# Optimization experiments

Hardware: AMD Instinct MI355X
Metric: run time of the kernel (lower is better)

Reference implementation:

```python
import jax, jax.numpy as jnp
import numpy as np

POS_THR = 0.5      # ROI_POSITIVE_THR
NEG_THR = 0.1      # ROI_NEGATIVE_THR
N_SAMPLES = 256    # ROI_SAMPLES
FG_RATIO = 0.25    # ROI_SAMPLE_RATIO
L1W = 1.0          # RPN.L1WEIGHT_INTERSECTION
NUM_FG = int(N_SAMPLES * FG_RATIO)


def _make_boxes(kxy, kwh, shape):
    # valid [x1,y1,x2,y2] boxes in an ~800px image
    xy = jax.random.uniform(kxy, shape[:-1] + (2,)) * 800.0
    wh = jax.random.uniform(kwh, shape[:-1] + (2,)) * 200.0 + 1.0
    return jnp.concatenate([xy, xy + wh], axis=-1)


def setup_inputs() -> dict:
    key = jax.random.key(0)
    k1, k2, k3, k4 = jax.random.split(key, 4)
    proposals = _make_boxes(k1, k2, (16, 16384, 4))  # [B, N, 4]
    gt_boxes = _make_boxes(k3, k4, (16, 128, 4))     # [B, G, 4]
    return {"proposals": proposals, "gt_boxes": gt_boxes}


def _centrehw(b):
    # [x1,y1,x2,y2] -> [cx,cy,w,h]
    x1, y1, x2, y2 = b[..., 0], b[..., 1], b[..., 2], b[..., 3]
    return jnp.stack([(x1 + x2) * 0.5, (y1 + y2) * 0.5, x2 - x1, y2 - y1], axis=-1)


def _targets(gt_c, roi_c):
    dx = (gt_c[..., 0] - roi_c[..., 0]) / roi_c[..., 2]
    dy = (gt_c[..., 1] - roi_c[..., 1]) / roi_c[..., 3]
    dw = jnp.log(gt_c[..., 2] / roi_c[..., 2])
    dh = jnp.log(gt_c[..., 3] / roi_c[..., 3])
    return jnp.stack([dx, dy, dw, dh], axis=-1)


def _iou(prop, gt):
    # prop [B,N,4], gt [B,G,4] -> IoU [B,N,G]
    p = prop[:, :, None, :]
    g = gt[:, None, :, :]
    ix1 = jnp.maximum(p[..., 0], g[..., 0])
    iy1 = jnp.maximum(p[..., 1], g[..., 1])
    ix2 = jnp.minimum(p[..., 2], g[..., 2])
    iy2 = jnp.minimum(p[..., 3], g[..., 3])
    inter = jnp.clip(ix2 - ix1, 0.0) * jnp.clip(iy2 - iy1, 0.0)
    ap = (p[..., 2] - p[..., 0]) * (p[..., 3] - p[..., 1])
    ag = (g[..., 2] - g[..., 0]) * (g[..., 3] - g[..., 1])
    return inter / jnp.maximum(ap + ag - inter, 1e-8)


def _forward(proposals, gt_boxes):
    B, N, _ = proposals.shape
    iou = _iou(proposals, gt_boxes)                       # [B,N,G]
    max_iou = iou.max(axis=-1)                            # [B,N]
    argmax_gt = iou.argmax(axis=-1).astype(jnp.int32)     # [B,N]
    # classify: 1=fg, 0=bg, -1=ignore
    labels = jnp.where(max_iou >= POS_THR, 1,
                       jnp.where(max_iou < NEG_THR, 0, -1)).astype(jnp.int32)
    # randsample: keep <= NUM_FG positives (random), fill rest with negatives.
    r = jax.random.uniform(jax.random.key(1), (B, N))
    pos = labels == 1
    r_pos = jnp.where(pos, r, -1.0)
    order = jnp.argsort(-r_pos, axis=1)
    ranks = jnp.argsort(order, axis=1)                    # rank among positives by r
    pos_sel = pos & (ranks < NUM_FG)
    prio = jnp.where(pos_sel, 3.0 + r,
                     jnp.where(labels == 0, 2.0 + r,
                               jnp.where(pos, 1.0 + r, r)))
    _, idx = jax.lax.top_k(prio, N_SAMPLES)               # [B,S] sampled proposal ids
    batch_labels = jnp.maximum(jnp.take_along_axis(labels, idx, axis=1), 0)  # [B,S]
    roi_batch = jnp.take_along_axis(proposals, idx[..., None], axis=1)       # [B,S,4]
    sel_gt = jnp.take_along_axis(argmax_gt, idx, axis=1)                     # [B,S]
    gt_batch = jnp.take_along_axis(gt_boxes, sel_gt[..., None], axis=1)      # [B,S,4]
    bbox_targets = _targets(_centrehw(gt_batch), _centrehw(roi_batch))       # [B,S,4]
    in_w = jnp.where((batch_labels == 1)[..., None], L1W, 0.0)
    in_w = jnp.broadcast_to(in_w, bbox_targets.shape)
    out_w = (in_w > 0).astype(jnp.float32)
    return roi_batch, batch_labels, bbox_targets, in_w, out_w


def reference(proposals, gt_boxes):
    return _forward(proposals, gt_boxes)
```

## Files before the change

kernel.cpp:

```cpp
#include <hip/hip_runtime.h>
#include <stdint.h>

#define BATCH 16
#define NPROP 16384
#define NGT   128
#define NSAMP 256
#define NFG   64
#define GCAP  512

__device__ __forceinline__ void thr_block(uint32_t c0, uint32_t c1,
                                          uint32_t* o0, uint32_t* o1) {
    const uint32_t k0 = 0u, k1 = 1u, ks2 = 0x1BD11BDBu;
    uint32_t x0 = c0 + k0, x1 = c1 + k1;
#define RND(d) { x0 += x1; x1 = (x1 << d) | (x1 >> (32 - d)); x1 ^= x0; }
    RND(13) RND(15) RND(26) RND(6)   x0 += k1;  x1 += ks2 + 1u;
    RND(17) RND(29) RND(16) RND(24)  x0 += ks2; x1 += k0 + 2u;
    RND(13) RND(15) RND(26) RND(6)   x0 += k0;  x1 += k1 + 3u;
    RND(17) RND(29) RND(16) RND(24)  x0 += k1;  x1 += ks2 + 4u;
    RND(13) RND(15) RND(26) RND(6)   x0 += ks2; x1 += k0 + 5u;
#undef RND
    *o0 = x0; *o1 = x1;
}

__device__ __forceinline__ uint32_t thr_part_xor(uint32_t f) {
    uint32_t a, b; thr_block(0u, f, &a, &b);
    return a ^ b;
}

__global__ void __launch_bounds__(256) k_compute(
    const float* __restrict__ props, const float* __restrict__ gts,
    uint32_t* __restrict__ packed)
{
#pragma clang fp contract(off)
    const int b = blockIdx.y;
    const int n = blockIdx.x * 256 + threadIdx.x;
    __shared__ float4 g4[NGT];
    if (threadIdx.x < NGT)
        g4[threadIdx.x] = ((const float4*)gts)[(size_t)b * NGT + threadIdx.x];
    __syncthreads();
    const float4 pb = ((const float4*)props)[(size_t)b * NPROP + n];
    const float ap = (pb.z - pb.x) * (pb.w - pb.y);
    float best = -1.0f; int bg = 0;
    #pragma unroll 4
    for (int i = 0; i < NGT; ++i) {
        const float4 gb = g4[i];
        float ag = (gb.z - gb.x) * (gb.w - gb.y);
        float w = fmaxf(fminf(pb.z, gb.z) - fmaxf(pb.x, gb.x), 0.0f);
        float h = fmaxf(fminf(pb.w, gb.w) - fmaxf(pb.y, gb.y), 0.0f);
        float inter = w * h;
        float un = fmaxf(ap + ag - inter, 1e-8f);
        float iou = inter / un;
        if (iou > best) { best = iou; bg = i; }
    }
    uint32_t lab = (best >= 0.5f) ? 2u : ((best < 0.1f) ? 1u : 0u);
    const uint32_t f = (uint32_t)b * NPROP + (uint32_t)n;
    packed[f] = ((thr_part_xor(f) >> 9) << 9) | (lab << 7) | (uint32_t)bg;
}

__device__ __forceinline__ float r_from_packed(uint32_t p) {
    return __uint_as_float(0x3F800000u | (p >> 9)) - 1.0f;
}

__device__ __forceinline__ uint64_t keyA(uint32_t p, uint32_t n) {
    return (((uint64_t)(p >> 9)) << 14) | (uint64_t)(16383u - n);
}
__device__ __forceinline__ uint32_t cls_of(uint32_t p, uint32_t n, uint64_t thrA) {
    uint32_t lab = (p >> 7) & 3u;
    if (lab == 2u) return (keyA(p, n) >= thrA) ? 3u : 1u;
    return (lab == 1u) ? 2u : 0u;
}
__device__ __forceinline__ uint64_t keyB(uint32_t p, uint32_t n, uint64_t thrA) {
    float r = r_from_packed(p);
    float prio = (float)cls_of(p, n, thrA) + r;
    return (((uint64_t)__float_as_uint(prio)) << 14) | (uint64_t)(16383u - n);
}

__global__ void __launch_bounds__(1024) k_select(
    const float* __restrict__ props, const float* __restrict__ gts,
    const uint32_t* __restrict__ packed, float* __restrict__ out)
{
#pragma clang fp contract(off)
    const int b = blockIdx.x;
    const int tid = threadIdx.x;
    __shared__ uint4 spk4[NPROP / 4];
    __shared__ uint32_t hist[2048];
    __shared__ uint64_t gat[GCAP];
    __shared__ uint32_t sh_pos, sh_neg, sel_cnt, gcnt;
    __shared__ uint32_t sh_dig, sh_k, sh_cnt_in;
    __shared__ uint64_t sh_thr;
    __shared__ uint64_t sel_keys[NSAMP];
    uint32_t* spk = (uint32_t*)spk4;

    const uint4* pk4 = (const uint4*)(packed + (size_t)b * NPROP);
    if (tid == 0) { sh_pos = 0; sh_neg = 0; sel_cnt = 0; }
    __syncthreads();
    {
        uint32_t cp = 0, cn = 0;
        #pragma unroll
        for (int i = 0; i < 4; i++) {
            uint4 v = pk4[tid + i * 1024];
            spk4[tid + i * 1024] = v;
            cp += (((v.x >> 7) & 3u) == 2u) + (((v.y >> 7) & 3u) == 2u)
                + (((v.z >> 7) & 3u) == 2u) + (((v.w >> 7) & 3u) == 2u);
            cn += (((v.x >> 7) & 3u) == 1u) + (((v.y >> 7) & 3u) == 1u)
                + (((v.z >> 7) & 3u) == 1u) + (((v.w >> 7) & 3u) == 1u);
        }
        #pragma unroll
        for (int off = 32; off > 0; off >>= 1) {
            cp += __shfl_down(cp, off);
            cn += __shfl_down(cn, off);
        }
        if ((tid & 63) == 0) { atomicAdd(&sh_pos, cp); atomicAdd(&sh_neg, cn); }
    }
    __syncthreads();
    const uint32_t npos = sh_pos;
    const uint32_t c3 = (npos < NFG) ? npos : NFG;
    const uint32_t c2 = sh_neg;
    const uint32_t c1 = npos - c3;

    uint64_t thrA = 0, thrB = 0;
    for (int phase = (npos > NFG ? 0 : 1); phase < 2; ++phase) {
        uint32_t k; int shift; uint32_t clsStar = 0;
        if (phase == 0) { k = NFG; shift = 26; }
        else {
            if (NSAMP <= c3 + c2)           { clsStar = 2; k = NSAMP - c3;           shift = 25; }
            else if (NSAMP <= c3 + c2 + c1) { clsStar = 1; k = NSAMP - c3 - c2;      shift = 26; }
            else                            { clsStar = 0; k = NSAMP - c3 - c2 - c1; shift = 34; }
        }
        uint64_t prefix = 0, mask = 0;
        for (;;) {
            hist[tid] = 0; hist[tid + 1024] = 0;
            __syncthreads();
            for (int i = 0; i < 16; i++) {
                uint32_t n = (uint32_t)(tid + i * 1024);
                uint32_t p = spk[n];
                bool elig; uint64_t key;
                if (phase == 0) { elig = (((p >> 7) & 3u) == 2u); key = keyA(p, n); }
                else { elig = (cls_of(p, n, thrA) == clsStar); key = keyB(p, n, thrA); }
                if (elig && ((key ^ prefix) & mask) == 0)
                    atomicAdd(&hist[(uint32_t)(key >> shift) & 2047u], 1u);
            }
            __syncthreads();
            if (tid < 64) {
                const uint32_t lane = tid;
                uint32_t cs = 0;
                if (lane < 32) {
                    const int base = (int)lane * 64;
                    #pragma unroll 8
                    for (int i = 0; i < 64; i++) cs += hist[base + i];
                }
                uint32_t s = cs;
                #pragma unroll
                for (int off = 1; off < 32; off <<= 1) {
                    uint32_t t = __shfl_down(s, off);
                    if (lane + off < 32) s += t;
                }
                uint32_t sExcl = s - cs;
                bool cond = (lane < 32) && (sExcl < k) && (k <= s);
                uint64_t ball = __ballot(cond);
                uint32_t cstar = (uint32_t)(__ffsll((unsigned long long)ball) - 1);
                uint32_t kc = __shfl(k - sExcl, (int)cstar);
                uint32_t val = hist[cstar * 64 + lane];
                uint32_t fi = val;
                #pragma unroll
                for (int off = 1; off < 64; off <<= 1) {
                    uint32_t t = __shfl_down(fi, off);
                    if (lane + off < 64) fi += t;
                }
                uint32_t fExcl = fi - val;
                bool cond2 = (fExcl < kc) && (kc <= fi);
                uint64_t ball2 = __ballot(cond2);
                uint32_t bstar = (uint32_t)(__ffsll((unsigned long long)ball2) - 1);
                if (lane == bstar) {
                    sh_dig = cstar * 64 + lane;
                    sh_k = kc - fExcl;
                    sh_cnt_in = val;
                }
            }
            __syncthreads();
            uint32_t dig = sh_dig, kk = sh_k, cnt = sh_cnt_in;
            prefix |= ((uint64_t)dig) << shift;
            mask   |= 2047ull << shift;
            if (cnt <= GCAP || shift == 0) {
                if (tid == 0) gcnt = 0;
                __syncthreads();
                for (int i = 0; i < 16; i++) {
                    uint32_t n = (uint32_t)(tid + i * 1024);
                    uint32_t p = spk[n];
                    bool elig; uint64_t key;
                    if (phase == 0) { elig = (((p >> 7) & 3u) == 2u); key = keyA(p, n); }
                    else { elig = (cls_of(p, n, thrA) == clsStar); key = keyB(p, n, thrA); }
                    if (elig && ((key ^ prefix) & mask) == 0) {
                        uint32_t s = atomicAdd(&gcnt, 1u);
                        if (s < GCAP) gat[s] = key;
                    }
                }
                __syncthreads();
                uint32_t gc = (gcnt < GCAP) ? gcnt : GCAP;
                if (tid < gc) {
                    uint64_t x = gat[tid];
                    uint32_t r = 0;
                    for (uint32_t j = 0; j < gc; j++) r += (gat[j] > x);
                    if (r == kk - 1) sh_thr = x;
                }
                __syncthreads();
                break;
            } else {
                k = kk;
                shift = (shift >= 11) ? shift - 11 : 0;
                __syncthreads();
            }
        }
        if (phase == 0) thrA = sh_thr; else thrB = sh_thr;
        __syncthreads();
    }

    for (int i = 0; i < 16; i++) {
        uint32_t n = (uint32_t)(tid + i * 1024);
        uint64_t key = keyB(spk[n], n, thrA);
        if (key >= thrB) {
            uint32_t slot = atomicAdd(&sel_cnt, 1u);
            if (slot < NSAMP) sel_keys[slot] = key;
        }
    }
    __syncthreads();

    if (tid < NSAMP) {
        uint64_t x = sel_keys[tid];
        uint32_t r = 0;
        for (int j = 0; j < NSAMP; j++) r += (sel_keys[j] > x);
        uint32_t n = 16383u - (uint32_t)(x & 0x3FFFu);
        uint32_t p = spk[n];
        uint32_t lab = (p >> 7) & 3u;
        uint32_t bg = p & 0x7Fu;
        const float4 pb = ((const float4*)props)[(size_t)b * NPROP + n];
        const float4 gb = ((const float4*)gts)[(size_t)b * NGT + bg];
        const size_t O_ROI = 0;
        const size_t O_LBL = (size_t)BATCH * NSAMP * 4;
        const size_t O_TGT = O_LBL + (size_t)BATCH * NSAMP;
        const size_t O_INW = O_TGT + (size_t)BATCH * NSAMP * 4;
        const size_t O_OUW = O_INW + (size_t)BATCH * NSAMP * 4;
        const size_t row = (size_t)b * NSAMP + r;
        out[O_ROI + row * 4 + 0] = pb.x;
        out[O_ROI + row * 4 + 1] = pb.y;
        out[O_ROI + row * 4 + 2] = pb.z;
        out[O_ROI + row * 4 + 3] = pb.w;
        const int isfg = (lab == 2u) ? 1 : 0;
        out[O_LBL + row] = isfg ? 1.0f : 0.0f;
        float rw  = pb.z - pb.x, rh = pb.w - pb.y;
        float gw  = gb.z - gb.x, gh = gb.w - gb.y;
        out[O_TGT + row * 4 + 0] = ((gb.x + gb.z) * 0.5f - (pb.x + pb.z) * 0.5f) / rw;
        out[O_TGT + row * 4 + 1] = ((gb.y + gb.w) * 0.5f - (pb.y + pb.w) * 0.5f) / rh;
        out[O_TGT + row * 4 + 2] = logf(gw / rw);
        out[O_TGT + row * 4 + 3] = logf(gh / rh);
        float wv = isfg ? 1.0f : 0.0f;
        for (int c = 0; c < 4; c++) {
            out[O_INW + row * 4 + c] = wv;
            out[O_OUW + row * 4 + c] = wv;
        }
    }
}

extern "C" void kernel_launch(void* const* d_in, const int* in_sizes, int n_in,
                              void* d_out, int out_size, void* d_ws, size_t ws_size,
                              hipStream_t stream) {
    (void)in_sizes; (void)n_in; (void)out_size; (void)ws_size;
    const float* props = (const float*)d_in[0];
    const float* gts   = (const float*)d_in[1];
    uint32_t* packed = (uint32_t*)d_ws;
    float* out = (float*)d_out;

    dim3 gridA(NPROP / 256, BATCH);
    k_compute<<<gridA, 256, 0, stream>>>(props, gts, packed);
    k_select<<<BATCH, 1024, 0, stream>>>(props, gts, packed, out);
}
```

Measured before the change: 108.1 us.

## Build first-pass radix histograms in compute kernel via global atomics

The IoU kernel now also builds per-batch 2048-bin histograms for the positive, negative and ignore classes using global atomics, so the select kernel can skip its first histogram pass and read counts directly. The select kernel no longer stages packed data in shared memory and reads it from global/L2 instead. The per-GT area is also precomputed once into shared memory. The cost is a memset plus 262k global atomics, and uncached repeated global reads in the later select passes.

```diff
diff --git a/kernel.cpp b/kernel.cpp
--- a/kernel.cpp
+++ b/kernel.cpp
@@ -29,14 +29,18 @@
 
 __global__ void __launch_bounds__(256) k_compute(
     const float* __restrict__ props, const float* __restrict__ gts,
-    uint32_t* __restrict__ packed)
+    uint32_t* __restrict__ packed, uint32_t* __restrict__ ghist)
 {
 #pragma clang fp contract(off)
     const int b = blockIdx.y;
     const int n = blockIdx.x * 256 + threadIdx.x;
     __shared__ float4 g4[NGT];
-    if (threadIdx.x < NGT)
-        g4[threadIdx.x] = ((const float4*)gts)[(size_t)b * NGT + threadIdx.x];
+    __shared__ float sag[NGT];
+    if (threadIdx.x < NGT) {
+        float4 g = ((const float4*)gts)[(size_t)b * NGT + threadIdx.x];
+        g4[threadIdx.x] = g;
+        sag[threadIdx.x] = (g.z - g.x) * (g.w - g.y);
+    }
     __syncthreads();
     const float4 pb = ((const float4*)props)[(size_t)b * NPROP + n];
     const float ap = (pb.z - pb.x) * (pb.w - pb.y);
@@ -44,17 +48,24 @@
     #pragma unroll 4
     for (int i = 0; i < NGT; ++i) {
         const float4 gb = g4[i];
-        float ag = (gb.z - gb.x) * (gb.w - gb.y);
         float w = fmaxf(fminf(pb.z, gb.z) - fmaxf(pb.x, gb.x), 0.0f);
-        float h = fmaxf(fminf(pb.w, gb.w) - fmaxf(pb.y, gb.y), 0.0f);
-        float inter = w * h;
-        float un = fmaxf(ap + ag - inter, 1e-8f);
+        float hh = fmaxf(fminf(pb.w, gb.w) - fmaxf(pb.y, gb.y), 0.0f);
+        float inter = w * hh;
+        float un = fmaxf(ap + sag[i] - inter, 1e-8f);
         float iou = inter / un;
         if (iou > best) { best = iou; bg = i; }
     }
     uint32_t lab = (best >= 0.5f) ? 2u : ((best < 0.1f) ? 1u : 0u);
     const uint32_t f = (uint32_t)b * NPROP + (uint32_t)n;
-    packed[f] = ((thr_part_xor(f) >> 9) << 9) | (lab << 7) | (uint32_t)bg;
+    uint32_t bits = thr_part_xor(f);
+    packed[f] = ((bits >> 9) << 9) | (lab << 7) | (uint32_t)bg;
+
+    float r = __uint_as_float(0x3F800000u | (bits >> 9)) - 1.0f;
+    uint32_t row, bucket;
+    if (lab == 2u)      { row = 0u; bucket = (bits >> 21) & 2047u; }
+    else if (lab == 1u) { row = 1u; bucket = (__float_as_uint(2.0f + r) >> 11) & 2047u; }
+    else                { row = 2u; bucket = (__float_as_uint(r) >> 20) & 2047u; }
+    atomicAdd(&ghist[(size_t)b * 6144 + row * 2048 + bucket], 1u);
 }
 
 __device__ __forceinline__ float r_from_packed(uint32_t p) {
@@ -77,33 +88,33 @@
 
 __global__ void __launch_bounds__(1024) k_select(
     const float* __restrict__ props, const float* __restrict__ gts,
-    const uint32_t* __restrict__ packed, float* __restrict__ out)
+    const uint32_t* __restrict__ packed, const uint32_t* __restrict__ ghist,
+    float* __restrict__ out)
 {
 #pragma clang fp contract(off)
     const int b = blockIdx.x;
     const int tid = threadIdx.x;
-    __shared__ uint4 spk4[NPROP / 4];
-    __shared__ uint32_t hist[2048];
+    __shared__ uint32_t h[3 * 2048];
+    __shared__ uint32_t hist2[2048];
     __shared__ uint64_t gat[GCAP];
+    __shared__ uint64_t sel_keys[NSAMP];
     __shared__ uint32_t sh_pos, sh_neg, sel_cnt, gcnt;
-    __shared__ uint32_t sh_dig, sh_k, sh_cnt_in;
+    __shared__ uint32_t sh_dig, sh_k, sh_cnt_in, sh_bA, sh_adjSub;
     __shared__ uint64_t sh_thr;
-    __shared__ uint64_t sel_keys[NSAMP];
-    uint32_t* spk = (uint32_t*)spk4;
-
-    const uint4* pk4 = (const uint4*)(packed + (size_t)b * NPROP);
+
+    const uint32_t* pk = packed + (size_t)b * NPROP;
+
     if (tid == 0) { sh_pos = 0; sh_neg = 0; sel_cnt = 0; }
     __syncthreads();
     {
         uint32_t cp = 0, cn = 0;
         #pragma unroll
-        for (int i = 0; i < 4; i++) {
-            uint4 v = pk4[tid + i * 1024];
-            spk4[tid + i * 1024] = v;
-            cp += (((v.x >> 7) & 3u) == 2u) + (((v.y >> 7) & 3u) == 2u)
-                + (((v.z >> 7) & 3u) == 2u) + (((v.w >> 7) & 3u) == 2u);
-            cn += (((v.x >> 7) & 3u) == 1u) + (((v.y >> 7) & 3u) == 1u)
-                + (((v.z >> 7) & 3u) == 1u) + (((v.w >> 7) & 3u) == 1u);
+        for (int i = 0; i < 6; i++) {
+            int idx = tid + i * 1024;
+            uint32_t v = ghist[(size_t)b * 6144 + idx];
+            h[idx] = v;
+            if (i < 2) cp += v;
+            else if (i < 4) cn += v;
         }
         #pragma unroll
         for (int off = 32; off > 0; off >>= 1) {
@@ -120,65 +131,79 @@
 
     uint64_t thrA = 0, thrB = 0;
     for (int phase = (npos > NFG ? 0 : 1); phase < 2; ++phase) {
-        uint32_t k; int shift; uint32_t clsStar = 0;
-        if (phase == 0) { k = NFG; shift = 26; }
+        uint32_t k; int shift; uint32_t clsStar = 0; const uint32_t* hrow;
+        if (phase == 0) { k = NFG; shift = 26; hrow = h; }
         else {
-            if (NSAMP <= c3 + c2)           { clsStar = 2; k = NSAMP - c3;           shift = 25; }
-            else if (NSAMP <= c3 + c2 + c1) { clsStar = 1; k = NSAMP - c3 - c2;      shift = 26; }
-            else                            { clsStar = 0; k = NSAMP - c3 - c2 - c1; shift = 34; }
+            if (NSAMP <= c3 + c2)           { clsStar = 2; k = NSAMP - c3;           shift = 25; hrow = h + 2048; }
+            else if (NSAMP <= c3 + c2 + c1) { clsStar = 1; k = NSAMP - c3 - c2;      shift = 26; hrow = h; }
+            else                            { clsStar = 0; k = NSAMP - c3 - c2 - c1; shift = 34; hrow = h + 4096; }
         }
         uint64_t prefix = 0, mask = 0;
+        bool first = true;
         for (;;) {
-            hist[tid] = 0; hist[tid + 1024] = 0;
-            __syncthreads();
-            for (int i = 0; i < 16; i++) {
-                uint32_t n = (uint32_t)(tid + i * 1024);
-                uint32_t p = spk[n];
-                bool elig; uint64_t key;
-                if (phase == 0) { elig = (((p >> 7) & 3u) == 2u); key = keyA(p, n); }
-                else { elig = (cls_of(p, n, thrA) == clsStar); key = keyB(p, n, thrA); }
-                if (elig && ((key ^ prefix) & mask) == 0)
-                    atomicAdd(&hist[(uint32_t)(key >> shift) & 2047u], 1u);
+            if (!first) {
+                hist2[tid] = 0; hist2[tid + 1024] = 0;
+                __syncthreads();
+                for (int i = 0; i < 16; i++) {
+                    uint32_t n = (uint32_t)(tid + i * 1024);
+                    uint32_t p = pk[n];
+                    bool elig; uint64_t key;
+                    if (phase == 0) { elig = (((p >> 7) & 3u) == 2u); key = keyA(p, n); }
+                    else { elig = (cls_of(p, n, thrA) == clsStar); key = keyB(p, n, thrA); }
+                    if (elig && ((key ^ prefix) & mask) == 0)
+                        atomicAdd(&hist2[(uint32_t)(key >> shift) & 2047u], 1u);
+                }
+                __syncthreads();
             }
-            __syncthreads();
-            if (tid < 64) {
-                const uint32_t lane = tid;
-                uint32_t cs = 0;
-                if (lane < 32) {
-                    const int base = (int)lane * 64;
-                    #pragma unroll 8
-                    for (int i = 0; i < 64; i++) cs += hist[base + i];
-                }
-                uint32_t s = cs;
-                #pragma unroll
-                for (int off = 1; off < 32; off <<= 1) {
-                    uint32_t t = __shfl_down(s, off);
-                    if (lane + off < 32) s += t;
-                }
-                uint32_t sExcl = s - cs;
-                bool cond = (lane < 32) && (sExcl < k) && (k <= s);
-                uint64_t ball = __ballot(cond);
-                uint32_t cstar = (uint32_t)(__ffsll((unsigned long long)ball) - 1);
-                uint32_t kc = __shfl(k - sExcl, (int)cstar);
-                uint32_t val = hist[cstar * 64 + lane];
-                uint32_t fi = val;
-                #pragma unroll
-                for (int off = 1; off < 64; off <<= 1) {
-                    uint32_t t = __shfl_down(fi, off);
-                    if (lane + off < 64) fi += t;
-                }
-                uint32_t fExcl = fi - val;
-                bool cond2 = (fExcl < kc) && (kc <= fi);
-                uint64_t ball2 = __ballot(cond2);
-                uint32_t bstar = (uint32_t)(__ffsll((unsigned long long)ball2) - 1);
-                if (lane == bstar) {
-                    sh_dig = cstar * 64 + lane;
-                    sh_k = kc - fExcl;
-                    sh_cnt_in = val;
+            {
+                const uint32_t* hsrc = first ? hrow : hist2;
+                const bool adj = first && (phase == 1) && (clsStar == 1u);
+                const uint32_t adjB = sh_bA, adjSub = sh_adjSub;
+                if (tid < 64) {
+                    const uint32_t lane = tid;
+                    auto HV = [&](uint32_t d) -> uint32_t {
+                        uint32_t v = hsrc[d];
+                        if (adj) v = (d > adjB) ? 0u : (d == adjB ? v - adjSub : v);
+                        return v;
+                    };
+                    uint32_t cs = 0;
+                    if (lane < 32) {
+                        const uint32_t base = lane * 64u;
+                        #pragma unroll 8
+                        for (uint32_t i = 0; i < 64; i++) cs += HV(base + i);
+                    }
+                    uint32_t s = cs;
+                    #pragma unroll
+                    for (int off = 1; off < 32; off <<= 1) {
+                        uint32_t t = __shfl_down(s, off);
+                        if (lane + off < 32) s += t;
+                    }
+                    uint32_t sExcl = s - cs;
+                    bool cond = (lane < 32) && (sExcl < k) && (k <= s);
+                    uint64_t ball = __ballot(cond);
+                    uint32_t cstar = (uint32_t)(__ffsll((unsigned long long)ball) - 1);
+                    uint32_t kc = __shfl(k - sExcl, (int)cstar);
+                    uint32_t val = HV(cstar * 64u + lane);
+                    uint32_t fi = val;
+                    #pragma unroll
+                    for (int off = 1; off < 64; off <<= 1) {
+                        uint32_t t = __shfl_down(fi, off);
+                        if (lane + off < 64) fi += t;
+                    }
+                    uint32_t fExcl = fi - val;
+                    bool cond2 = (fExcl < kc) && (kc <= fi);
+                    uint64_t ball2 = __ballot(cond2);
+                    uint32_t bstar = (uint32_t)(__ffsll((unsigned long long)ball2) - 1);
+                    if (lane == bstar) {
+                        sh_dig = cstar * 64u + lane;
+                        sh_k = kc - fExcl;
+                        sh_cnt_in = val;
+                    }
                 }
             }
             __syncthreads();
             uint32_t dig = sh_dig, kk = sh_k, cnt = sh_cnt_in;
+            if (phase == 0 && first && tid == 0) { sh_bA = dig; sh_adjSub = kk; }
             prefix |= ((uint64_t)dig) << shift;
             mask   |= 2047ull << shift;
             if (cnt <= GCAP || shift == 0) {
@@ -186,7 +211,7 @@
                 __syncthreads();
                 for (int i = 0; i < 16; i++) {
                     uint32_t n = (uint32_t)(tid + i * 1024);
-                    uint32_t p = spk[n];
+                    uint32_t p = pk[n];
                     bool elig; uint64_t key;
                     if (phase == 0) { elig = (((p >> 7) & 3u) == 2u); key = keyA(p, n); }
                     else { elig = (cls_of(p, n, thrA) == clsStar); key = keyB(p, n, thrA); }
@@ -197,7 +222,7 @@
                 }
                 __syncthreads();
                 uint32_t gc = (gcnt < GCAP) ? gcnt : GCAP;
-                if (tid < gc) {
+                if (tid < (int)gc) {
                     uint64_t x = gat[tid];
                     uint32_t r = 0;
                     for (uint32_t j = 0; j < gc; j++) r += (gat[j] > x);
@@ -208,6 +233,7 @@
             } else {
                 k = kk;
                 shift = (shift >= 11) ? shift - 11 : 0;
+                first = false;
                 __syncthreads();
             }
         }
@@ -217,7 +243,7 @@
 
     for (int i = 0; i < 16; i++) {
         uint32_t n = (uint32_t)(tid + i * 1024);
-        uint64_t key = keyB(spk[n], n, thrA);
+        uint64_t key = keyB(pk[n], n, thrA);
         if (key >= thrB) {
             uint32_t slot = atomicAdd(&sel_cnt, 1u);
             if (slot < NSAMP) sel_keys[slot] = key;
@@ -230,7 +256,7 @@
         uint32_t r = 0;
         for (int j = 0; j < NSAMP; j++) r += (sel_keys[j] > x);
         uint32_t n = 16383u - (uint32_t)(x & 0x3FFFu);
-        uint32_t p = spk[n];
+        uint32_t p = pk[n];
         uint32_t lab = (p >> 7) & 3u;
         uint32_t bg = p & 0x7Fu;
         const float4 pb = ((const float4*)props)[(size_t)b * NPROP + n];
@@ -268,9 +294,11 @@
     const float* props = (const float*)d_in[0];
     const float* gts   = (const float*)d_in[1];
     uint32_t* packed = (uint32_t*)d_ws;
+    uint32_t* ghist  = packed + (size_t)BATCH * NPROP;
     float* out = (float*)d_out;
 
+    hipMemsetAsync(ghist, 0, (size_t)BATCH * 3 * 2048 * sizeof(uint32_t), stream);
     dim3 gridA(NPROP / 256, BATCH);
-    k_compute<<<gridA, 256, 0, stream>>>(props, gts, packed);
-    k_select<<<BATCH, 1024, 0, stream>>>(props, gts, packed, out);
-}
+    k_compute<<<gridA, 256, 0, stream>>>(props, gts, packed, ghist);
+    k_select<<<BATCH, 1024, 0, stream>>>(props, gts, packed, ghist, out);
+}
```

New measurement: 146.1 us. +35.2%, slower.

## Compact pos/neg proposals into per-batch lists and split IoU across thread pairs

Applied to the files above, without the earlier changes.

The compute kernel now splits the 128 GT comparisons across two threads per proposal and precomputes GT areas in shared memory. It also stream-compacts proposals into a per-batch 64-bit entry list, with fg/bg at the front and ignored ones at the back, using wave ballots and global atomic counters. The select kernel then runs its radix top-k only over the compacted front list held in LDS, instead of scanning all 16384 entries per phase. This adds a zeroing kernel launch, global atomics and nondeterministic list order, and a global-memory fallback when the list exceeds LDS capacity.

```diff
diff --git a/kernel.cpp b/kernel.cpp
--- a/kernel.cpp
+++ b/kernel.cpp
@@ -7,6 +7,9 @@
 #define NSAMP 256
 #define NFG   64
 #define GCAP  512
+#define LCAP  8192
+
+typedef unsigned long long ull;
 
 __device__ __forceinline__ void thr_block(uint32_t c0, uint32_t c1,
                                           uint32_t* o0, uint32_t* o1) {
@@ -27,212 +30,258 @@
     return a ^ b;
 }
 
+__global__ void k_zero(uint32_t* c) {
+    if (threadIdx.x < 48) c[threadIdx.x] = 0u;
+}
+
 __global__ void __launch_bounds__(256) k_compute(
     const float* __restrict__ props, const float* __restrict__ gts,
-    uint32_t* __restrict__ packed)
+    ull* __restrict__ lists, uint32_t* __restrict__ cnts)
 {
 #pragma clang fp contract(off)
     const int b = blockIdx.y;
-    const int n = blockIdx.x * 256 + threadIdx.x;
+    const int tid = threadIdx.x;
+    const int half = tid & 1;
+    const int n = blockIdx.x * 128 + (tid >> 1);
     __shared__ float4 g4[NGT];
-    if (threadIdx.x < NGT)
-        g4[threadIdx.x] = ((const float4*)gts)[(size_t)b * NGT + threadIdx.x];
+    __shared__ float sag[NGT];
+    if (tid < NGT) {
+        float4 g = ((const float4*)gts)[(size_t)b * NGT + tid];
+        g4[tid] = g;
+        sag[tid] = (g.z - g.x) * (g.w - g.y);
+    }
     __syncthreads();
     const float4 pb = ((const float4*)props)[(size_t)b * NPROP + n];
     const float ap = (pb.z - pb.x) * (pb.w - pb.y);
     float best = -1.0f; int bg = 0;
+    const int gbase = half << 6;
     #pragma unroll 4
-    for (int i = 0; i < NGT; ++i) {
-        const float4 gb = g4[i];
-        float ag = (gb.z - gb.x) * (gb.w - gb.y);
-        float w = fmaxf(fminf(pb.z, gb.z) - fmaxf(pb.x, gb.x), 0.0f);
-        float h = fmaxf(fminf(pb.w, gb.w) - fmaxf(pb.y, gb.y), 0.0f);
-        float inter = w * h;
-        float un = fmaxf(ap + ag - inter, 1e-8f);
+    for (int i = 0; i < 64; ++i) {
+        const int gi = gbase + i;
+        const float4 gb = g4[gi];
+        float w  = fmaxf(fminf(pb.z, gb.z) - fmaxf(pb.x, gb.x), 0.0f);
+        float hh = fmaxf(fminf(pb.w, gb.w) - fmaxf(pb.y, gb.y), 0.0f);
+        float inter = w * hh;
+        float un = fmaxf(ap + sag[gi] - inter, 1e-8f);
         float iou = inter / un;
-        if (iou > best) { best = iou; bg = i; }
-    }
+        if (iou > best) { best = iou; bg = gi; }
+    }
+    float ob = __shfl_xor(best, 1);
+    int  obg = __shfl_xor(bg, 1);
+    if ((tid & 1) == 0 && ob > best) { best = ob; bg = obg; }
+
     uint32_t lab = (best >= 0.5f) ? 2u : ((best < 0.1f) ? 1u : 0u);
     const uint32_t f = (uint32_t)b * NPROP + (uint32_t)n;
-    packed[f] = ((thr_part_xor(f) >> 9) << 9) | (lab << 7) | (uint32_t)bg;
-}
-
-__device__ __forceinline__ float r_from_packed(uint32_t p) {
-    return __uint_as_float(0x3F800000u | (p >> 9)) - 1.0f;
-}
-
-__device__ __forceinline__ uint64_t keyA(uint32_t p, uint32_t n) {
-    return (((uint64_t)(p >> 9)) << 14) | (uint64_t)(16383u - n);
-}
-__device__ __forceinline__ uint32_t cls_of(uint32_t p, uint32_t n, uint64_t thrA) {
-    uint32_t lab = (p >> 7) & 3u;
-    if (lab == 2u) return (keyA(p, n) >= thrA) ? 3u : 1u;
-    return (lab == 1u) ? 2u : 0u;
-}
-__device__ __forceinline__ uint64_t keyB(uint32_t p, uint32_t n, uint64_t thrA) {
-    float r = r_from_packed(p);
-    float prio = (float)cls_of(p, n, thrA) + r;
-    return (((uint64_t)__float_as_uint(prio)) << 14) | (uint64_t)(16383u - n);
+    uint32_t mant = thr_part_xor(f) >> 9;
+    ull entry = ((ull)(lab == 2u) << 44) | ((ull)mant << 21)
+              | ((ull)(16383u - (uint32_t)n) << 7) | (ull)(uint32_t)bg;
+
+    const bool isEven = (tid & 1) == 0;
+    bool front = isEven && (lab != 0u);
+    bool back  = isEven && (lab == 0u);
+    bool ispos = isEven && (lab == 2u);
+    ull mF = __ballot(front), mB = __ballot(back), mP = __ballot(ispos);
+    uint32_t lane = (uint32_t)tid & 63u;
+    ull lt = lane ? (~0ull >> (64u - lane)) : 0ull;
+    uint32_t bf = 0, bb = 0;
+    if (lane == 0) {
+        if (mF) bf = atomicAdd(&cnts[b],      (uint32_t)__popcll(mF));
+        if (mB) bb = atomicAdd(&cnts[16 + b], (uint32_t)__popcll(mB));
+        if (mP)      atomicAdd(&cnts[32 + b], (uint32_t)__popcll(mP));
+    }
+    bf = (uint32_t)__shfl((int)bf, 0);
+    bb = (uint32_t)__shfl((int)bb, 0);
+    ull* Lb = lists + (size_t)b * NPROP;
+    if (front) Lb[bf + (uint32_t)__popcll(mF & lt)] = entry;
+    if (back)  Lb[16383u - (bb + (uint32_t)__popcll(mB & lt))] = entry;
 }
 
 __global__ void __launch_bounds__(1024) k_select(
     const float* __restrict__ props, const float* __restrict__ gts,
-    const uint32_t* __restrict__ packed, float* __restrict__ out)
+    const ull* __restrict__ lists, const uint32_t* __restrict__ cnts,
+    float* __restrict__ out)
 {
 #pragma clang fp contract(off)
     const int b = blockIdx.x;
     const int tid = threadIdx.x;
-    __shared__ uint4 spk4[NPROP / 4];
+    __shared__ ull      sf[LCAP];
     __shared__ uint32_t hist[2048];
-    __shared__ uint64_t gat[GCAP];
-    __shared__ uint32_t sh_pos, sh_neg, sel_cnt, gcnt;
-    __shared__ uint32_t sh_dig, sh_k, sh_cnt_in;
-    __shared__ uint64_t sh_thr;
-    __shared__ uint64_t sel_keys[NSAMP];
-    uint32_t* spk = (uint32_t*)spk4;
-
-    const uint4* pk4 = (const uint4*)(packed + (size_t)b * NPROP);
-    if (tid == 0) { sh_pos = 0; sh_neg = 0; sel_cnt = 0; }
+    __shared__ ull      gat[GCAP];
+    __shared__ ull      selk[NSAMP];
+    __shared__ uint32_t sela[NSAMP];
+    __shared__ uint32_t sh_dig, sh_k, sh_cnt_in, gcnt, selc;
+    __shared__ ull sh_thr;
+
+    const ull* Lb = lists + (size_t)b * NPROP;
+    const uint32_t npn  = cnts[b];
+    const uint32_t nig  = cnts[16 + b];
+    const uint32_t npos = cnts[32 + b];
+    const bool inLDS = (npn <= LCAP);
+    if (inLDS) for (uint32_t j = tid; j < npn; j += 1024) sf[j] = Lb[j];
+    if (tid == 0) selc = 0;
     __syncthreads();
-    {
-        uint32_t cp = 0, cn = 0;
-        #pragma unroll
-        for (int i = 0; i < 4; i++) {
-            uint4 v = pk4[tid + i * 1024];
-            spk4[tid + i * 1024] = v;
-            cp += (((v.x >> 7) & 3u) == 2u) + (((v.y >> 7) & 3u) == 2u)
-                + (((v.z >> 7) & 3u) == 2u) + (((v.w >> 7) & 3u) == 2u);
-            cn += (((v.x >> 7) & 3u) == 1u) + (((v.y >> 7) & 3u) == 1u)
-                + (((v.z >> 7) & 3u) == 1u) + (((v.w >> 7) & 3u) == 1u);
-        }
-        #pragma unroll
-        for (int off = 32; off > 0; off >>= 1) {
-            cp += __shfl_down(cp, off);
-            cn += __shfl_down(cn, off);
-        }
-        if ((tid & 63) == 0) { atomicAdd(&sh_pos, cp); atomicAdd(&sh_neg, cn); }
-    }
-    __syncthreads();
-    const uint32_t npos = sh_pos;
-    const uint32_t c3 = (npos < NFG) ? npos : NFG;
-    const uint32_t c2 = sh_neg;
-    const uint32_t c1 = npos - c3;
-
-    uint64_t thrA = 0, thrB = 0;
-    for (int phase = (npos > NFG ? 0 : 1); phase < 2; ++phase) {
-        uint32_t k; int shift; uint32_t clsStar = 0;
-        if (phase == 0) { k = NFG; shift = 26; }
-        else {
-            if (NSAMP <= c3 + c2)           { clsStar = 2; k = NSAMP - c3;           shift = 25; }
-            else if (NSAMP <= c3 + c2 + c1) { clsStar = 1; k = NSAMP - c3 - c2;      shift = 26; }
-            else                            { clsStar = 0; k = NSAMP - c3 - c2 - c1; shift = 34; }
-        }
-        uint64_t prefix = 0, mask = 0;
+
+    auto getF = [&](uint32_t j) -> ull { return inLDS ? sf[j] : Lb[j]; };
+    auto keyA_of = [&](ull e) -> ull {
+        return (((e >> 21) & 0x7FFFFFull) << 14) | ((e >> 7) & 0x3FFFull);
+    };
+
+    auto locate = [&](uint32_t k) {
+        if (tid < 64) {
+            const uint32_t lane = (uint32_t)tid;
+            uint32_t cs = 0;
+            if (lane < 32) {
+                const uint32_t base = lane * 64u;
+                #pragma unroll 8
+                for (uint32_t i = 0; i < 64; i++) cs += hist[base + i];
+            }
+            uint32_t s = cs;
+            #pragma unroll
+            for (int off = 1; off < 32; off <<= 1) {
+                uint32_t t = __shfl_down(s, off);
+                if (lane + off < 32) s += t;
+            }
+            uint32_t sExcl = s - cs;
+            bool cond = (lane < 32) && (sExcl < k) && (k <= s);
+            ull ball = __ballot(cond);
+            uint32_t cstar = (uint32_t)(__ffsll((unsigned long long)ball) - 1);
+            uint32_t kc = (uint32_t)__shfl((int)(k - sExcl), (int)cstar);
+            uint32_t val = hist[cstar * 64u + lane];
+            uint32_t fi = val;
+            #pragma unroll
+            for (int off = 1; off < 64; off <<= 1) {
+                uint32_t t = __shfl_down(fi, off);
+                if (lane + off < 64) fi += t;
+            }
+            uint32_t fExcl = fi - val;
+            bool cond2 = (fExcl < kc) && (kc <= fi);
+            ull ball2 = __ballot(cond2);
+            uint32_t bstar = (uint32_t)(__ffsll((unsigned long long)ball2) - 1);
+            if (lane == bstar) {
+                sh_dig = cstar * 64u + lane;
+                sh_k = kc - fExcl;
+                sh_cnt_in = val;
+            }
+        }
+    };
+
+    auto radix = [&](auto&& kf, uint32_t m, uint32_t k, int shift) -> ull {
+        ull prefix = 0, mask = 0;
         for (;;) {
             hist[tid] = 0; hist[tid + 1024] = 0;
             __syncthreads();
-            for (int i = 0; i < 16; i++) {
-                uint32_t n = (uint32_t)(tid + i * 1024);
-                uint32_t p = spk[n];
-                bool elig; uint64_t key;
-                if (phase == 0) { elig = (((p >> 7) & 3u) == 2u); key = keyA(p, n); }
-                else { elig = (cls_of(p, n, thrA) == clsStar); key = keyB(p, n, thrA); }
-                if (elig && ((key ^ prefix) & mask) == 0)
+            for (uint32_t j = tid; j < m; j += 1024) {
+                bool e; ull key = kf(j, e);
+                if (e && ((key ^ prefix) & mask) == 0)
                     atomicAdd(&hist[(uint32_t)(key >> shift) & 2047u], 1u);
             }
             __syncthreads();
-            if (tid < 64) {
-                const uint32_t lane = tid;
-                uint32_t cs = 0;
-                if (lane < 32) {
-                    const int base = (int)lane * 64;
-                    #pragma unroll 8
-                    for (int i = 0; i < 64; i++) cs += hist[base + i];
-                }
-                uint32_t s = cs;
-                #pragma unroll
-                for (int off = 1; off < 32; off <<= 1) {
-                    uint32_t t = __shfl_down(s, off);
-                    if (lane + off < 32) s += t;
-                }
-                uint32_t sExcl = s - cs;
-                bool cond = (lane < 32) && (sExcl < k) && (k <= s);
-                uint64_t ball = __ballot(cond);
-                uint32_t cstar = (uint32_t)(__ffsll((unsigned long long)ball) - 1);
-                uint32_t kc = __shfl(k - sExcl, (int)cstar);
-                uint32_t val = hist[cstar * 64 + lane];
-                uint32_t fi = val;
-                #pragma unroll
-                for (int off = 1; off < 64; off <<= 1) {
-                    uint32_t t = __shfl_down(fi, off);
-                    if (lane + off < 64) fi += t;
-                }
-                uint32_t fExcl = fi - val;
-                bool cond2 = (fExcl < kc) && (kc <= fi);
-                uint64_t ball2 = __ballot(cond2);
-                uint32_t bstar = (uint32_t)(__ffsll((unsigned long long)ball2) - 1);
-                if (lane == bstar) {
-                    sh_dig = cstar * 64 + lane;
-                    sh_k = kc - fExcl;
-                    sh_cnt_in = val;
-                }
-            }
+            locate(k);
             __syncthreads();
             uint32_t dig = sh_dig, kk = sh_k, cnt = sh_cnt_in;
-            prefix |= ((uint64_t)dig) << shift;
+            prefix |= ((ull)dig) << shift;
             mask   |= 2047ull << shift;
             if (cnt <= GCAP || shift == 0) {
                 if (tid == 0) gcnt = 0;
                 __syncthreads();
-                for (int i = 0; i < 16; i++) {
-                    uint32_t n = (uint32_t)(tid + i * 1024);
-                    uint32_t p = spk[n];
-                    bool elig; uint64_t key;
-                    if (phase == 0) { elig = (((p >> 7) & 3u) == 2u); key = keyA(p, n); }
-                    else { elig = (cls_of(p, n, thrA) == clsStar); key = keyB(p, n, thrA); }
-                    if (elig && ((key ^ prefix) & mask) == 0) {
+                for (uint32_t j = tid; j < m; j += 1024) {
+                    bool e; ull key = kf(j, e);
+                    if (e && ((key ^ prefix) & mask) == 0) {
                         uint32_t s = atomicAdd(&gcnt, 1u);
                         if (s < GCAP) gat[s] = key;
                     }
                 }
                 __syncthreads();
                 uint32_t gc = (gcnt < GCAP) ? gcnt : GCAP;
-                if (tid < gc) {
-                    uint64_t x = gat[tid];
+                if (tid < (int)gc) {
+                    ull x = gat[tid];
                     uint32_t r = 0;
                     for (uint32_t j = 0; j < gc; j++) r += (gat[j] > x);
                     if (r == kk - 1) sh_thr = x;
                 }
                 __syncthreads();
-                break;
+                return sh_thr;
             } else {
                 k = kk;
                 shift = (shift >= 11) ? shift - 11 : 0;
                 __syncthreads();
             }
         }
-        if (phase == 0) thrA = sh_thr; else thrB = sh_thr;
-        __syncthreads();
-    }
-
-    for (int i = 0; i < 16; i++) {
-        uint32_t n = (uint32_t)(tid + i * 1024);
-        uint64_t key = keyB(spk[n], n, thrA);
-        if (key >= thrB) {
-            uint32_t slot = atomicAdd(&sel_cnt, 1u);
-            if (slot < NSAMP) sel_keys[slot] = key;
-        }
+    };
+
+    ull thrA = 0;
+    if (npos > NFG) {
+        thrA = radix([&](uint32_t j, bool& e) -> ull {
+            ull ent = getF(j);
+            e = ((ent >> 44) & 1ull) != 0;
+            return keyA_of(ent);
+        }, npn, NFG, 26);
+    }
+
+    auto keyB_of = [&](ull ent) -> ull {
+        uint32_t mant = (uint32_t)((ent >> 21) & 0x7FFFFFull);
+        uint32_t invn = (uint32_t)((ent >> 7) & 0x3FFFull);
+        float r = __uint_as_float(0x3F800000u | mant) - 1.0f;
+        uint32_t cls;
+        if ((ent >> 44) & 1ull) cls = (keyA_of(ent) >= thrA) ? 3u : 1u;
+        else cls = 2u;
+        float prio = (float)cls + r;
+        return (((ull)__float_as_uint(prio)) << 14) | (ull)invn;
+    };
+    auto key0_of = [&](ull ent) -> ull {
+        uint32_t mant = (uint32_t)((ent >> 21) & 0x7FFFFFull);
+        uint32_t invn = (uint32_t)((ent >> 7) & 0x3FFFull);
+        float r = __uint_as_float(0x3F800000u | mant) - 1.0f;
+        float prio = 0.0f + r;
+        return (((ull)__float_as_uint(prio)) << 14) | (ull)invn;
+    };
+
+    ull thrB = 0, thr0 = 0;
+    uint32_t needIgn = 0;
+    if (npn >= NSAMP) {
+        thrB = radix([&](uint32_t j, bool& e) -> ull { e = true; return keyB_of(getF(j)); },
+                     npn, NSAMP, 34);
+    } else {
+        needIgn = NSAMP - npn;
+        thr0 = radix([&](uint32_t j, bool& e) -> ull { e = true; return key0_of(Lb[16383u - j]); },
+                     nig, needIgn, 34);
     }
     __syncthreads();
 
+    for (uint32_t j = tid; j < npn; j += 1024) {
+        ull ent = getF(j);
+        ull key = keyB_of(ent);
+        if (npn < NSAMP || key >= thrB) {
+            uint32_t s = atomicAdd(&selc, 1u);
+            if (s < NSAMP) {
+                selk[s] = key;
+                sela[s] = ((uint32_t)((ent >> 44) & 1ull) << 7) | (uint32_t)(ent & 0x7Full);
+            }
+        }
+    }
+    if (needIgn) {
+        for (uint32_t j = tid; j < nig; j += 1024) {
+            ull ent = Lb[16383u - j];
+            ull key = key0_of(ent);
+            if (key >= thr0) {
+                uint32_t s = atomicAdd(&selc, 1u);
+                if (s < NSAMP) {
+                    selk[s] = key;
+                    sela[s] = (uint32_t)(ent & 0x7Full);
+                }
+            }
+        }
+    }
+    __syncthreads();
+
     if (tid < NSAMP) {
-        uint64_t x = sel_keys[tid];
+        ull x = selk[tid];
         uint32_t r = 0;
-        for (int j = 0; j < NSAMP; j++) r += (sel_keys[j] > x);
-        uint32_t n = 16383u - (uint32_t)(x & 0x3FFFu);
-        uint32_t p = spk[n];
-        uint32_t lab = (p >> 7) & 3u;
-        uint32_t bg = p & 0x7Fu;
+        for (int j = 0; j < NSAMP; j++) r += (selk[j] > x);
+        uint32_t n = 16383u - (uint32_t)(x & 0x3FFFull);
+        uint32_t aux = sela[tid];
+        uint32_t bg = aux & 0x7Fu;
+        const int isfg = (int)((aux >> 7) & 1u);
         const float4 pb = ((const float4*)props)[(size_t)b * NPROP + n];
         const float4 gb = ((const float4*)gts)[(size_t)b * NGT + bg];
         const size_t O_ROI = 0;
@@ -245,7 +294,6 @@
         out[O_ROI + row * 4 + 1] = pb.y;
         out[O_ROI + row * 4 + 2] = pb.z;
         out[O_ROI + row * 4 + 3] = pb.w;
-        const int isfg = (lab == 2u) ? 1 : 0;
         out[O_LBL + row] = isfg ? 1.0f : 0.0f;
         float rw  = pb.z - pb.x, rh = pb.w - pb.y;
         float gw  = gb.z - gb.x, gh = gb.w - gb.y;
@@ -267,10 +315,12 @@
     (void)in_sizes; (void)n_in; (void)out_size; (void)ws_size;
     const float* props = (const float*)d_in[0];
     const float* gts   = (const float*)d_in[1];
-    uint32_t* packed = (uint32_t*)d_ws;
+    ull* lists = (ull*)d_ws;
+    uint32_t* cnts = (uint32_t*)((char*)d_ws + (size_t)BATCH * NPROP * 8);
     float* out = (float*)d_out;
 
-    dim3 gridA(NPROP / 256, BATCH);
-    k_compute<<<gridA, 256, 0, stream>>>(props, gts, packed);
-    k_select<<<BATCH, 1024, 0, stream>>>(props, gts, packed, out);
-}
+    k_zero<<<1, 64, 0, stream>>>(cnts);
+    dim3 gridA(NPROP / 128, BATCH);
+    k_compute<<<gridA, 256, 0, stream>>>(props, gts, lists, cnts);
+    k_select<<<BATCH, 1024, 0, stream>>>(props, gts, lists, cnts, out);
+}
```

After: 298.0 us. 176% more time.
